# Kernel optimization log

Hardware: AMD Instinct MI355X
Metric: run time of the kernel (lower is better)

## Reference

```python
import jax, jax.numpy as jnp
import numpy as np


def setup_inputs() -> dict:
    key = jax.random.key(0)
    k1, k2, k3 = jax.random.split(key, 3)
    x = jax.random.normal(k1, (8, 256, 160, 160), dtype=jnp.float32)
    # conv weights: OIHW layout, Kaiming-ish scale
    w7 = jax.random.normal(k2, (1, 2, 7, 7), dtype=jnp.float32) * (1.0 / np.sqrt(2 * 7 * 7))
    w3 = jax.random.normal(k3, (1, 2, 3, 3), dtype=jnp.float32) * (1.0 / np.sqrt(2 * 3 * 3))
    alpha = jnp.asarray(0.5, dtype=jnp.float32)
    return {"x": x, "w7": w7, "w3": w3, "alpha": alpha}


def _conv_same(desc, w, pad):
    # desc: [B, 2, H, W], w: [1, 2, k, k] -> [B, 1, H, W]
    return jax.lax.conv_general_dilated(
        desc, w, window_strides=(1, 1), padding=[(pad, pad), (pad, pad)],
        dimension_numbers=("NCHW", "OIHW", "NCHW"))


def reference(x, w7, w3, alpha):
    avg = jnp.mean(x, axis=1, keepdims=True)          # [B,1,H,W]
    mx = jnp.max(x, axis=1, keepdims=True)            # [B,1,H,W]
    desc = jnp.concatenate([avg, mx], axis=1)         # [B,2,H,W]
    a7 = _conv_same(desc, w7, 3)
    a3 = _conv_same(desc, w3, 1)
    w = jax.nn.sigmoid(alpha * a7 + (1.0 - alpha) * a3)
    return x * w
```

## Files before the change

kernel.cpp:

```cpp
#include <hip/hip_runtime.h>
#include <float.h>
#include <math.h>

#define Bn 8
#define Cn 256
#define Hn 160
#define Wn 160
#define HWn (Hn * Wn)
#define NPIX (Bn * HWn)
#define NTOT (Bn * Cn * HWn)

typedef float v4f __attribute__((ext_vector_type(4)));

__global__ __launch_bounds__(256) void k_reduce(const float* __restrict__ x,
                                                float* __restrict__ avgp,
                                                float* __restrict__ maxp) {
    const int tid  = threadIdx.x;
    const int lane = tid & 63;
    const int wv   = tid >> 6;
    const int base = blockIdx.x << 8;
    const int b    = base / HWn;
    const int hwb  = base - b * HWn;
    const float* xp = x + (size_t)b * Cn * HWn + hwb + (lane << 2);
    const int c0 = wv << 6;

    float4 s = make_float4(0.f, 0.f, 0.f, 0.f);
    float4 m = make_float4(-FLT_MAX, -FLT_MAX, -FLT_MAX, -FLT_MAX);
    #pragma unroll 8
    for (int c = 0; c < 64; ++c) {
        const float4 v = *reinterpret_cast<const float4*>(xp + (size_t)(c0 + c) * HWn);
        s.x += v.x; s.y += v.y; s.z += v.z; s.w += v.w;
        m.x = fmaxf(m.x, v.x); m.y = fmaxf(m.y, v.y);
        m.z = fmaxf(m.z, v.z); m.w = fmaxf(m.w, v.w);
    }

    __shared__ float4 ss[4][64];
    __shared__ float4 sm[4][64];
    ss[wv][lane] = s;
    sm[wv][lane] = m;
    __syncthreads();

    if (tid < 64) {
        const float4 s0 = ss[0][tid], s1 = ss[1][tid], s2 = ss[2][tid], s3 = ss[3][tid];
        const float4 m0 = sm[0][tid], m1 = sm[1][tid], m2 = sm[2][tid], m3 = sm[3][tid];
        const float inv = 1.0f / (float)Cn;
        float4 av, mx;
        av.x = (s0.x + s1.x + s2.x + s3.x) * inv;
        av.y = (s0.y + s1.y + s2.y + s3.y) * inv;
        av.z = (s0.z + s1.z + s2.z + s3.z) * inv;
        av.w = (s0.w + s1.w + s2.w + s3.w) * inv;
        mx.x = fmaxf(fmaxf(m0.x, m1.x), fmaxf(m2.x, m3.x));
        mx.y = fmaxf(fmaxf(m0.y, m1.y), fmaxf(m2.y, m3.y));
        mx.z = fmaxf(fmaxf(m0.z, m1.z), fmaxf(m2.z, m3.z));
        mx.w = fmaxf(fmaxf(m0.w, m1.w), fmaxf(m2.w, m3.w));
        reinterpret_cast<float4*>(avgp)[(base >> 2) + tid] = av;
        reinterpret_cast<float4*>(maxp)[(base >> 2) + tid] = mx;
    }
}

__global__ __launch_bounds__(256) void k_conv(const float* __restrict__ avgp,
                                              const float* __restrict__ maxp,
                                              const float* __restrict__ w7,
                                              const float* __restrict__ w3,
                                              const float* __restrict__ alphap,
                                              float* __restrict__ wmap) {
    const int p  = blockIdx.x * 256 + threadIdx.x;
    const int b  = p / HWn;
    const int hw = p - b * HWn;
    const int h  = hw / Wn;
    const int w  = hw - h * Wn;
    const float* ap = avgp + b * HWn;
    const float* mp = maxp + b * HWn;

    float a7 = 0.f;
    #pragma unroll
    for (int kh = 0; kh < 7; ++kh) {
        const int hh = h + kh - 3;
        if (hh < 0 || hh >= Hn) continue;
        #pragma unroll
        for (int kw = 0; kw < 7; ++kw) {
            const int ww = w + kw - 3;
            if (ww < 0 || ww >= Wn) continue;
            const int o = hh * Wn + ww;
            a7 = fmaf(ap[o], w7[kh * 7 + kw], a7);
            a7 = fmaf(mp[o], w7[49 + kh * 7 + kw], a7);
        }
    }

    float a3 = 0.f;
    #pragma unroll
    for (int kh = 0; kh < 3; ++kh) {
        const int hh = h + kh - 1;
        if (hh < 0 || hh >= Hn) continue;
        #pragma unroll
        for (int kw = 0; kw < 3; ++kw) {
            const int ww = w + kw - 1;
            if (ww < 0 || ww >= Wn) continue;
            const int o = hh * Wn + ww;
            a3 = fmaf(ap[o], w3[kh * 3 + kw], a3);
            a3 = fmaf(mp[o], w3[9 + kh * 3 + kw], a3);
        }
    }

    const float alpha = *alphap;
    const float z = alpha * a7 + (1.0f - alpha) * a3;
    wmap[p] = 1.0f / (1.0f + expf(-z));
}

__global__ __launch_bounds__(256) void k_mul(const float* __restrict__ x,
                                             const float* __restrict__ wmap,
                                             float* __restrict__ out) {
    const int n4   = NTOT / 4;
    const int chw4 = (Cn * HWn) / 4;
    const int hw4  = HWn / 4;
    const int stride = gridDim.x * blockDim.x;
    for (int i = blockIdx.x * blockDim.x + threadIdx.x; i < n4; i += stride) {
        const int b  = i / chw4;
        const int r  = i - b * chw4;
        const int hw = r % hw4;
        const v4f xv = *(reinterpret_cast<const v4f*>(x) + i);
        const float4 wv = reinterpret_cast<const float4*>(wmap)[b * hw4 + hw];
        v4f o;
        o.x = xv.x * wv.x;
        o.y = xv.y * wv.y;
        o.z = xv.z * wv.z;
        o.w = xv.w * wv.w;
        __builtin_nontemporal_store(o, reinterpret_cast<v4f*>(out) + i);
    }
}

extern "C" void kernel_launch(void* const* d_in, const int* in_sizes, int n_in,
                              void* d_out, int out_size, void* d_ws, size_t ws_size,
                              hipStream_t stream) {
    const float* x      = (const float*)d_in[0];
    const float* w7     = (const float*)d_in[1];
    const float* w3     = (const float*)d_in[2];
    const float* alphap = (const float*)d_in[3];
    float* out = (float*)d_out;

    float* avgp = (float*)d_ws;
    float* maxp = avgp + NPIX;
    float* wmap = maxp + NPIX;

    k_reduce<<<NPIX / 256, 256, 0, stream>>>(x, avgp, maxp);
    k_conv<<<NPIX / 256, 256, 0, stream>>>(avgp, maxp, w7, w3, alphap, wmap);
    k_mul<<<4096, 256, 0, stream>>>(x, wmap, out);
}
```

Measured before the change: 112.0 us.

## Fuse conv/sigmoid map computation into the broadcast multiply kernel

Merges the conv kernel and the multiply kernel. Each 256-pixel block computes its sigmoid attention weights into shared memory, then streams all 256 channels of x for those pixels and writes the scaled output. This drops the wmap global round trip and one kernel launch, and uses nontemporal loads for x. The cost is that conv work now sits at the start of every multiply block, and access is a strided per-channel walk rather than the grid-stride linear sweep.

New measurement: 114.9 us. +2.6%, slower.

```diff
diff --git a/kernel.cpp b/kernel.cpp
--- a/kernel.cpp
+++ b/kernel.cpp
@@ -9,6 +9,9 @@
 #define HWn (Hn * Wn)
 #define NPIX (Bn * HWn)
 #define NTOT (Bn * Cn * HWn)
+#define PBLK 256
+#define BLKS (NPIX / PBLK)
+#define BPB  (HWn / PBLK)
 
 typedef float v4f __attribute__((ext_vector_type(4)));
 
@@ -58,74 +61,79 @@
     }
 }
 
-__global__ __launch_bounds__(256) void k_conv(const float* __restrict__ avgp,
-                                              const float* __restrict__ maxp,
-                                              const float* __restrict__ w7,
-                                              const float* __restrict__ w3,
-                                              const float* __restrict__ alphap,
-                                              float* __restrict__ wmap) {
-    const int p  = blockIdx.x * 256 + threadIdx.x;
-    const int b  = p / HWn;
-    const int hw = p - b * HWn;
-    const int h  = hw / Wn;
-    const int w  = hw - h * Wn;
-    const float* ap = avgp + b * HWn;
-    const float* mp = maxp + b * HWn;
+__global__ __launch_bounds__(256) void k_convmul(const float* __restrict__ x,
+                                                 const float* __restrict__ avgp,
+                                                 const float* __restrict__ maxp,
+                                                 const float* __restrict__ w7,
+                                                 const float* __restrict__ w3,
+                                                 const float* __restrict__ alphap,
+                                                 float* __restrict__ out) {
+    __shared__ float w_lds[PBLK];
 
-    float a7 = 0.f;
-    #pragma unroll
-    for (int kh = 0; kh < 7; ++kh) {
-        const int hh = h + kh - 3;
-        if (hh < 0 || hh >= Hn) continue;
+    const int tid  = threadIdx.x;
+    const int base = blockIdx.x << 8;
+    const int b    = base / HWn;
+    const int hwb  = base - b * HWn;
+
+    {
+        const int hw = hwb + tid;
+        const int h  = hw / Wn;
+        const int w  = hw - h * Wn;
+        const float* ap = avgp + b * HWn;
+        const float* mp = maxp + b * HWn;
+
+        float a7 = 0.f;
         #pragma unroll
-        for (int kw = 0; kw < 7; ++kw) {
-            const int ww = w + kw - 3;
-            if (ww < 0 || ww >= Wn) continue;
-            const int o = hh * Wn + ww;
-            a7 = fmaf(ap[o], w7[kh * 7 + kw], a7);
-            a7 = fmaf(mp[o], w7[49 + kh * 7 + kw], a7);
+        for (int kh = 0; kh < 7; ++kh) {
+            const int hh = h + kh - 3;
+            if (hh < 0 || hh >= Hn) continue;
+            #pragma unroll
+            for (int kw = 0; kw < 7; ++kw) {
+                const int ww = w + kw - 3;
+                if (ww < 0 || ww >= Wn) continue;
+                const int o = hh * Wn + ww;
+                a7 = fmaf(ap[o], w7[kh * 7 + kw], a7);
+                a7 = fmaf(mp[o], w7[49 + kh * 7 + kw], a7);
+            }
         }
+
+        float a3 = 0.f;
+        #pragma unroll
+        for (int kh = 0; kh < 3; ++kh) {
+            const int hh = h + kh - 1;
+            if (hh < 0 || hh >= Hn) continue;
+            #pragma unroll
+            for (int kw = 0; kw < 3; ++kw) {
+                const int ww = w + kw - 1;
+                if (ww < 0 || ww >= Wn) continue;
+                const int o = hh * Wn + ww;
+                a3 = fmaf(ap[o], w3[kh * 3 + kw], a3);
+                a3 = fmaf(mp[o], w3[9 + kh * 3 + kw], a3);
+            }
+        }
+
+        const float alpha = *alphap;
+        const float z = alpha * a7 + (1.0f - alpha) * a3;
+        w_lds[tid] = 1.0f / (1.0f + expf(-z));
     }
+    __syncthreads();
 
-    float a3 = 0.f;
-    #pragma unroll
-    for (int kh = 0; kh < 3; ++kh) {
-        const int hh = h + kh - 1;
-        if (hh < 0 || hh >= Hn) continue;
-        #pragma unroll
-        for (int kw = 0; kw < 3; ++kw) {
-            const int ww = w + kw - 1;
-            if (ww < 0 || ww >= Wn) continue;
-            const int o = hh * Wn + ww;
-            a3 = fmaf(ap[o], w3[kh * 3 + kw], a3);
-            a3 = fmaf(mp[o], w3[9 + kh * 3 + kw], a3);
-        }
-    }
+    const int lane = tid & 63;
+    const int wv   = tid >> 6;
+    const int c0   = wv << 6;
 
-    const float alpha = *alphap;
-    const float z = alpha * a7 + (1.0f - alpha) * a3;
-    wmap[p] = 1.0f / (1.0f + expf(-z));
-}
+    const float4 wf = reinterpret_cast<const float4*>(w_lds)[lane];
+    const v4f wvf = { wf.x, wf.y, wf.z, wf.w };
 
-__global__ __launch_bounds__(256) void k_mul(const float* __restrict__ x,
-                                             const float* __restrict__ wmap,
-                                             float* __restrict__ out) {
-    const int n4   = NTOT / 4;
-    const int chw4 = (Cn * HWn) / 4;
-    const int hw4  = HWn / 4;
-    const int stride = gridDim.x * blockDim.x;
-    for (int i = blockIdx.x * blockDim.x + threadIdx.x; i < n4; i += stride) {
-        const int b  = i / chw4;
-        const int r  = i - b * chw4;
-        const int hw = r % hw4;
-        const v4f xv = *(reinterpret_cast<const v4f*>(x) + i);
-        const float4 wv = reinterpret_cast<const float4*>(wmap)[b * hw4 + hw];
-        v4f o;
-        o.x = xv.x * wv.x;
-        o.y = xv.y * wv.y;
-        o.z = xv.z * wv.z;
-        o.w = xv.w * wv.w;
-        __builtin_nontemporal_store(o, reinterpret_cast<v4f*>(out) + i);
+    const size_t off0 = (size_t)b * Cn * HWn + hwb + (lane << 2);
+    const v4f* __restrict__ xin = reinterpret_cast<const v4f*>(x + off0);
+    v4f* __restrict__ oout = reinterpret_cast<v4f*>(out + off0);
+
+    #pragma unroll 8
+    for (int c = 0; c < 64; ++c) {
+        const size_t idx = ((size_t)(c0 + c) * HWn) >> 2;
+        const v4f xv = __builtin_nontemporal_load(xin + idx);
+        __builtin_nontemporal_store(xv * wvf, oout + idx);
     }
 }
 
@@ -140,9 +148,7 @@
 
     float* avgp = (float*)d_ws;
     float* maxp = avgp + NPIX;
-    float* wmap = maxp + NPIX;
 
-    k_reduce<<<NPIX / 256, 256, 0, stream>>>(x, avgp, maxp);
-    k_conv<<<NPIX / 256, 256, 0, stream>>>(avgp, maxp, w7, w3, alphap, wmap);
-    k_mul<<<4096, 256, 0, stream>>>(x, wmap, out);
+    k_reduce <<<BLKS, 256, 0, stream>>>(x, avgp, maxp);
+    k_convmul<<<BLKS, 256, 0, stream>>>(x, avgp, maxp, w7, w3, alphap, out);
 }
```

## Split channel reduction across more blocks with 64 pixels per block

Applied to the files above, without the earlier changes.

The channel-reduction kernel now handles 64 pixels per block instead of 256. Each wave splits its lanes into 4 channel groups of 16 lanes, so 16 channel slices are reduced in parallel and combined through shared memory. This launches 4x more blocks and cuts each thread's serial load chain from 64 to 16, aiming for more memory-level parallelism on the read of x. The multiply kernel's grid is also halved. The cost is shorter contiguous reads per channel row (256 bytes instead of 1 KB) and a longer final reduction step.

New measurement: 118.2 us. +5.5%, slower.

```diff
diff --git a/kernel.cpp b/kernel.cpp
--- a/kernel.cpp
+++ b/kernel.cpp
@@ -9,6 +9,8 @@
 #define HWn (Hn * Wn)
 #define NPIX (Bn * HWn)
 #define NTOT (Bn * Cn * HWn)
+#define PPB 64
+#define RBLKS (NPIX / PPB)
 
 typedef float v4f __attribute__((ext_vector_type(4)));
 
@@ -18,43 +20,48 @@
     const int tid  = threadIdx.x;
     const int lane = tid & 63;
     const int wv   = tid >> 6;
-    const int base = blockIdx.x << 8;
+    const int g    = lane & 15;
+    const int cs   = lane >> 4;
+    const int base = blockIdx.x * PPB;
     const int b    = base / HWn;
     const int hwb  = base - b * HWn;
-    const float* xp = x + (size_t)b * Cn * HWn + hwb + (lane << 2);
-    const int c0 = wv << 6;
+    const float* xp = x + (size_t)b * Cn * HWn + hwb + (g << 2);
+    const int c0 = (wv << 2) + cs;
 
     float4 s = make_float4(0.f, 0.f, 0.f, 0.f);
     float4 m = make_float4(-FLT_MAX, -FLT_MAX, -FLT_MAX, -FLT_MAX);
-    #pragma unroll 8
-    for (int c = 0; c < 64; ++c) {
-        const float4 v = *reinterpret_cast<const float4*>(xp + (size_t)(c0 + c) * HWn);
+    #pragma unroll
+    for (int k = 0; k < 16; ++k) {
+        const int c = (k << 4) + c0;
+        const float4 v = *reinterpret_cast<const float4*>(xp + (size_t)c * HWn);
         s.x += v.x; s.y += v.y; s.z += v.z; s.w += v.w;
         m.x = fmaxf(m.x, v.x); m.y = fmaxf(m.y, v.y);
         m.z = fmaxf(m.z, v.z); m.w = fmaxf(m.w, v.w);
     }
 
-    __shared__ float4 ss[4][64];
-    __shared__ float4 sm[4][64];
-    ss[wv][lane] = s;
-    sm[wv][lane] = m;
+    __shared__ float4 ss[16][16];
+    __shared__ float4 sm[16][16];
+    const int p = (wv << 2) + cs;
+    ss[p][g] = s;
+    sm[p][g] = m;
     __syncthreads();
 
-    if (tid < 64) {
-        const float4 s0 = ss[0][tid], s1 = ss[1][tid], s2 = ss[2][tid], s3 = ss[3][tid];
-        const float4 m0 = sm[0][tid], m1 = sm[1][tid], m2 = sm[2][tid], m3 = sm[3][tid];
+    if (tid < 16) {
+        float4 as = ss[0][tid];
+        float4 am = sm[0][tid];
+        #pragma unroll
+        for (int q = 1; q < 16; ++q) {
+            const float4 qs = ss[q][tid];
+            const float4 qm = sm[q][tid];
+            as.x += qs.x; as.y += qs.y; as.z += qs.z; as.w += qs.w;
+            am.x = fmaxf(am.x, qm.x); am.y = fmaxf(am.y, qm.y);
+            am.z = fmaxf(am.z, qm.z); am.w = fmaxf(am.w, qm.w);
+        }
         const float inv = 1.0f / (float)Cn;
-        float4 av, mx;
-        av.x = (s0.x + s1.x + s2.x + s3.x) * inv;
-        av.y = (s0.y + s1.y + s2.y + s3.y) * inv;
-        av.z = (s0.z + s1.z + s2.z + s3.z) * inv;
-        av.w = (s0.w + s1.w + s2.w + s3.w) * inv;
-        mx.x = fmaxf(fmaxf(m0.x, m1.x), fmaxf(m2.x, m3.x));
-        mx.y = fmaxf(fmaxf(m0.y, m1.y), fmaxf(m2.y, m3.y));
-        mx.z = fmaxf(fmaxf(m0.z, m1.z), fmaxf(m2.z, m3.z));
-        mx.w = fmaxf(fmaxf(m0.w, m1.w), fmaxf(m2.w, m3.w));
+        float4 av;
+        av.x = as.x * inv; av.y = as.y * inv; av.z = as.z * inv; av.w = as.w * inv;
         reinterpret_cast<float4*>(avgp)[(base >> 2) + tid] = av;
-        reinterpret_cast<float4*>(maxp)[(base >> 2) + tid] = mx;
+        reinterpret_cast<float4*>(maxp)[(base >> 2) + tid] = am;
     }
 }
 
@@ -142,7 +149,7 @@
     float* maxp = avgp + NPIX;
     float* wmap = maxp + NPIX;
 
-    k_reduce<<<NPIX / 256, 256, 0, stream>>>(x, avgp, maxp);
-    k_conv<<<NPIX / 256, 256, 0, stream>>>(avgp, maxp, w7, w3, alphap, wmap);
-    k_mul<<<4096, 256, 0, stream>>>(x, wmap, out);
+    k_reduce<<<RBLKS,      256, 0, stream>>>(x, avgp, maxp);
+    k_conv  <<<NPIX / 256, 256, 0, stream>>>(avgp, maxp, w7, w3, alphap, wmap);
+    k_mul   <<<2048,       256, 0, stream>>>(x, wmap, out);
 }
```
